# Kernel tuning notes

Hardware: AMD Instinct MI355X
Metric: run time of the kernel (lower is better)

Reference implementation:

```python
import jax, jax.numpy as jnp
import numpy as np

N = 12  # mmse_block_size
REAL_SIZE = N * (N + 1) // 2  # 78: diag + strict lower
IMAG_SIZE = N * (N - 1) // 2  # 66: strict lower only
ROWS, COLS = jnp.tril_indices(N)        # row-major (i, j<=i) matches torch loop order
ROWS_S, COLS_S = jnp.tril_indices(N, -1)  # strict lower, row-major, matches imag loop
DIAG_MASK = jnp.eye(N, dtype=bool)


def _mlp(x, W1, b1, W2, b2, W3, b3):
    h = jax.nn.relu(x @ W1 + b1)
    h = jax.nn.relu(h @ W2 + b2)
    return h @ W3 + b3


def _cholesky_outer(flat):
    # flat: [B, REAL_SIZE + IMAG_SIZE] -> [B, N, N] complex, L @ L^H
    B = flat.shape[0]
    L_real = jnp.zeros((B, N, N), flat.dtype).at[:, ROWS, COLS].set(flat[:, :REAL_SIZE])
    L_real = jnp.where(DIAG_MASK, jax.nn.softplus(L_real), L_real)
    L_imag = jnp.zeros((B, N, N), flat.dtype).at[:, ROWS_S, COLS_S].set(
        flat[:, REAL_SIZE:REAL_SIZE + IMAG_SIZE])
    L = L_real + 1j * L_imag
    return jnp.einsum('bij,bkj->bik', L, jnp.conj(L))


def setup_inputs() -> dict:
    key = jax.random.key(0)
    ks = jax.random.split(key, 13)
    L, H, OUT = 4096, 64, REAL_SIZE + IMAG_SIZE
    sc = lambda k, shp, fan: (jax.random.normal(k, shp, jnp.float32) / np.sqrt(fan))
    return {
        'channel_stats': jax.random.normal(ks[0], (8192, L), jnp.float32),
        'WC1': sc(ks[1], (L, H), L), 'bC1': jnp.zeros((H,), jnp.float32),
        'WC2': sc(ks[2], (H, H), H), 'bC2': jnp.zeros((H,), jnp.float32),
        'WC3': sc(ks[3], (H, OUT), H), 'bC3': jnp.zeros((OUT,), jnp.float32),
        'WR1': sc(ks[4], (L, H), L), 'bR1': jnp.zeros((H,), jnp.float32),
        'WR2': sc(ks[5], (H, H), H), 'bR2': jnp.zeros((H,), jnp.float32),
        'WR3': sc(ks[6], (H, OUT), H), 'bR3': jnp.zeros((OUT,), jnp.float32),
    }


def reference(channel_stats, WC1, bC1, WC2, bC2, WC3, bC3,
              WR1, bR1, WR2, bR2, WR3, bR3):
    C_flat = _mlp(channel_stats, WC1, bC1, WC2, bC2, WC3, bC3)
    R_flat = _mlp(channel_stats, WR1, bR1, WR2, bR2, WR3, bR3)
    C = _cholesky_outer(C_flat)
    R = _cholesky_outer(R_flat)
    return C, R
```

## Files before the change

### kernel.cpp

```cpp
#include <hip/hip_runtime.h>
#include <stdint.h>

#define M_ROWS 8192
#define K_DIM  4096
#define OUTD   144
#define PLANE  1179648
#define KCH    8
#define NSTEP  8

typedef __attribute__((ext_vector_type(4))) float  float4v;
typedef __attribute__((ext_vector_type(8))) short  short8v;

static __device__ __forceinline__ unsigned short f2bf(float f) {
    unsigned int u = __builtin_bit_cast(unsigned int, f);
    u += 0x7FFFu + ((u >> 16) & 1u);
    return (unsigned short)(u >> 16);
}

__global__ __launch_bounds__(256) void wt_kernel(
    const float* __restrict__ WC1, const float* __restrict__ WR1,
    unsigned short* __restrict__ Wt) {
    __shared__ float tile[64][65];
    const float* src = (blockIdx.y == 0) ? WC1 : WR1;
    const int k0 = blockIdx.x * 64;
    const int t = threadIdx.x;
    const int j = t & 63, qq = t >> 6;
#pragma unroll
    for (int p = 0; p < 16; ++p) {
        int i = p * 4 + qq;
        tile[i][j] = src[(size_t)(k0 + i) * 64 + j];
    }
    __syncthreads();
    const int tt  = blockIdx.x >> 1;
    const int ksb = (blockIdx.x & 1) * 2;
#pragma unroll
    for (int p = 0; p < 16; ++p) {
        int c = p * 256 + t;
        int e = c & 7, m = (c >> 3) & 15, q = (c >> 7) & 3;
        int ks_l = (c >> 9) & 1, w_l = (c >> 10) & 3;
        int kp = ks_l * 32 + q * 8 + e;
        int np = w_l * 16 + m;
        int wg = blockIdx.y * 4 + w_l;
        size_t dst = ((size_t)(wg * 32 + tt) * 4 + (ksb + ks_l)) * 512
                   + q * 128 + m * 8 + e;
        Wt[dst] = f2bf(tile[kp][np]);
    }
}


#define ISSUE_AX(S_, X0_, X1_, X2_, X3_)                       \
    do { const float* ap_ = xpw + (S_) * 64;                   \
         X0_ = *(const float4*)(ap_);                          \
         X1_ = *(const float4*)(ap_ + 4);                      \
         X2_ = *(const float4*)(ap_ + 32);                     \
         X3_ = *(const float4*)(ap_ + 36); } while (0)

#define STORE_AX(BUF_, X0_, X1_, X2_, X3_)                             \
    do { short8v s1_, s2_;                                             \
         s1_[0] = (short)f2bf((X0_).x); s1_[1] = (short)f2bf((X0_).y); \
         s1_[2] = (short)f2bf((X0_).z); s1_[3] = (short)f2bf((X0_).w); \
         s1_[4] = (short)f2bf((X1_).x); s1_[5] = (short)f2bf((X1_).y); \
         s1_[6] = (short)f2bf((X1_).z); s1_[7] = (short)f2bf((X1_).w); \
         s2_[0] = (short)f2bf((X2_).x); s2_[1] = (short)f2bf((X2_).y); \
         s2_[2] = (short)f2bf((X2_).z); s2_[3] = (short)f2bf((X2_).w); \
         s2_[4] = (short)f2bf((X3_).x); s2_[5] = (short)f2bf((X3_).y); \
         s2_[6] = (short)f2bf((X3_).z); s2_[7] = (short)f2bf((X3_).w); \
         *(short8v*)(awp + (BUF_) * 8192) = s1_;                       \
         *(short8v*)(awp + (BUF_) * 8192 + 512) = s2_; } while (0)

#define ISSUE_B2(S_, B0_, B1_)                                   \
    do { const unsigned short* bp_ = bpw + (size_t)(2 * (S_)) * 512; \
         B0_ = *(const short8v*)(bp_);                           \
         B1_ = *(const short8v*)(bp_ + 512); } while (0)

#define MFR2(BUF_, B0_, B1_)                                                   \
    do { _Pragma("unroll")                                                     \
         for (int rb = 0; rb < 8; ++rb) {                                      \
             const unsigned short* ab_ = Asm_ + (BUF_) * 8192 + rb * 1024 + lane * 8; \
             short8v a0_ = *(const short8v*)(ab_);                             \
             short8v a1_ = *(const short8v*)(ab_ + 512);                       \
             acc[rb] = __builtin_amdgcn_mfma_f32_16x16x32_bf16(a0_, B0_, acc[rb], 0, 0, 0); \
             acc[rb] = __builtin_amdgcn_mfma_f32_16x16x32_bf16(a1_, B1_, acc[rb], 0, 0, 0); \
         } } while (0)

__global__ __launch_bounds__(512, 4) void gemm1_kernel(
    const float* __restrict__ X, const unsigned short* __restrict__ Wt,
    float* __restrict__ PART) {
    __shared__ __align__(16) unsigned short Asm_[2 * 8192];

    const int tid  = threadIdx.x;
    const int lane = tid & 63;
    const int w    = tid >> 6;
    const int m    = lane & 15, q = lane >> 4;
    const int mt   = blockIdx.x & 63;
    const int kc   = blockIdx.x >> 6;
    const int r0   = mt * 128;

    const int srow = tid & 127, sq8 = tid >> 7;
    const float* xpw = X + (size_t)(r0 + srow) * K_DIM + kc * 512 + sq8 * 8;
    unsigned short* awp = Asm_ + (srow >> 4) * 1024 + (16 * sq8 + (srow & 15)) * 8;

    const unsigned short* bpw = Wt + (size_t)(w * 128 + kc * 16) * 512 + lane * 8;

    float4v acc[8];
#pragma unroll
    for (int rb = 0; rb < 8; ++rb) acc[rb] = (float4v){0.f, 0.f, 0.f, 0.f};

    float4 xa0, xa1, xa2, xa3;
    short8v bA0, bA1, bB0, bB1;

    ISSUE_AX(0, xa0, xa1, xa2, xa3);
    ISSUE_B2(0, bA0, bA1);

#pragma unroll 1
    for (int sp = 0; sp < NSTEP / 2; ++sp) {
        const int s = sp * 2;
        STORE_AX(0, xa0, xa1, xa2, xa3);
        ISSUE_AX(s + 1, xa0, xa1, xa2, xa3);
        asm volatile("s_waitcnt lgkmcnt(0)" ::: "memory");
        __builtin_amdgcn_s_barrier();
        __builtin_amdgcn_sched_barrier(0);
        ISSUE_B2(s + 1, bB0, bB1);
        MFR2(0, bA0, bA1);
        STORE_AX(1, xa0, xa1, xa2, xa3);
        if (s + 2 < NSTEP) ISSUE_AX(s + 2, xa0, xa1, xa2, xa3);
        asm volatile("s_waitcnt lgkmcnt(0)" ::: "memory");
        __builtin_amdgcn_s_barrier();
        __builtin_amdgcn_sched_barrier(0);
        if (s + 2 < NSTEP) ISSUE_B2(s + 2, bA0, bA1);
        MFR2(1, bB0, bB1);
    }

    {
        float* Pf = PART + (size_t)kc * (M_ROWS * 128);
        const int col = w * 16 + m;
#pragma unroll
        for (int rb = 0; rb < 8; ++rb)
#pragma unroll
            for (int i = 0; i < 4; ++i) {
                int grow = r0 + rb * 16 + q * 4 + i;
                Pf[(size_t)grow * 128 + col] = acc[rb][i];
            }
    }
}

__global__ __launch_bounds__(512, 6) void tail_kernel(
    const float* __restrict__ PART,
    const float* __restrict__ bC1, const float* __restrict__ bR1,
    const float* __restrict__ WC2, const float* __restrict__ bC2,
    const float* __restrict__ WR2, const float* __restrict__ bR2,
    const float* __restrict__ WC3, const float* __restrict__ bC3,
    const float* __restrict__ WR3, const float* __restrict__ bR3,
    unsigned int* __restrict__ O32) {
    __shared__ __align__(16) char smem[41216];
    float* hs  = (float*)smem;
    float* W2s = hs + 16 * 132;
    float* fl  = W2s;

    const int tid = threadIdx.x;
    const int r0  = blockIdx.x * 16;

    {
        int r = tid >> 5, c4 = tid & 31;
        const float* p0 = PART + (size_t)(r0 + r) * 128 + c4 * 4;
        float4 s = *(const float4*)(p0);
#pragma unroll
        for (int kc = 1; kc < KCH; ++kc) {
            float4 v = *(const float4*)(p0 + (size_t)kc * (M_ROWS * 128));
            s.x += v.x; s.y += v.y; s.z += v.z; s.w += v.w;
        }
        int c = c4 * 4;
        const float* bsrc = (c < 64) ? (bC1 + c) : (bR1 + (c - 64));
        s.x += bsrc[0]; s.y += bsrc[1]; s.z += bsrc[2]; s.w += bsrc[3];
        s.x = s.x > 0.f ? s.x : 0.f;  s.y = s.y > 0.f ? s.y : 0.f;
        s.z = s.z > 0.f ? s.z : 0.f;  s.w = s.w > 0.f ? s.w : 0.f;
        *(float4*)&hs[r * 132 + c] = s;
    }
#pragma unroll
    for (int p = 0; p < 4; ++p) {
        int fi = p * 512 + tid;
        int k = fi >> 5, c4 = fi & 31;
        int c = c4 * 4;
        const float* wsrc = (c < 64) ? (WC2 + (size_t)k * 64 + c)
                                     : (WR2 + (size_t)k * 64 + (c - 64));
        *(float4*)&W2s[k * 128 + c] = *(const float4*)wsrc;
    }
    __syncthreads();

    const int rg = tid >> 5;
    const int cg = tid & 31;
    const int koff2 = (cg < 16) ? 0 : 64;
    float acc2[4];
    {
        int c = cg * 4;
        const float* bsrc = (c < 64) ? (bC2 + c) : (bR2 + (c - 64));
#pragma unroll
        for (int j = 0; j < 4; ++j) acc2[j] = bsrc[j];
    }
    for (int k = 0; k < 64; ++k) {
        float4 wv = *(const float4*)&W2s[k * 128 + cg * 4];
        float a = hs[rg * 132 + koff2 + k];
        acc2[0] += a * wv.x; acc2[1] += a * wv.y;
        acc2[2] += a * wv.z; acc2[3] += a * wv.w;
    }
    float4 h2v;
    h2v.x = acc2[0] > 0.f ? acc2[0] : 0.f;
    h2v.y = acc2[1] > 0.f ? acc2[1] : 0.f;
    h2v.z = acc2[2] > 0.f ? acc2[2] : 0.f;
    h2v.w = acc2[3] > 0.f ? acc2[3] : 0.f;
    __syncthreads();
    *(float4*)&hs[rg * 132 + cg * 4] = h2v;
    __syncthreads();

#pragma unroll 1
    for (int pass = 0; pass < 3; ++pass) {
        int c = pass * 128 + cg * 4;
        if (c < 288) {
            const int brn = (c >= 144);
            const int cl = c - (brn ? 144 : 0);
            const float* W3 = brn ? WR3 : WC3;
            const float* b3 = brn ? bR3 : bC3;
            const int ko = brn ? 64 : 0;
            float a3[4];
#pragma unroll
            for (int j = 0; j < 4; ++j) a3[j] = b3[cl + j];
            for (int k = 0; k < 64; ++k) {
                float4 wv = *(const float4*)(W3 + (size_t)k * OUTD + cl);
                float a = hs[rg * 132 + ko + k];
                a3[0] += a * wv.x; a3[1] += a * wv.y;
                a3[2] += a * wv.z; a3[3] += a * wv.w;
            }
            float4 v; v.x = a3[0]; v.y = a3[1]; v.z = a3[2]; v.w = a3[3];
            *(float4*)&fl[rg * 288 + c] = v;
        }
    }
    __syncthreads();

    if (tid < 384) {
        int r = tid / 24, rem = tid % 24;
        int brn = rem / 12, ii = rem % 12;
        float* f = &fl[r * 288 + brn * 144];
        int d = ii * (ii + 1) / 2 + ii;
        float xv = f[d];
        f[d] = (xv > 20.f) ? xv : log1pf(expf(xv));
    }
    __syncthreads();

    for (int task = tid; task < 16 * 2 * 78; task += 512) {
        int r = task / 156, rem = task % 156;
        int brn = rem / 78, p = rem % 78;
        int i = 0;
        while (p >= (i + 1) * (i + 2) / 2) ++i;
        int j = p - i * (i + 1) / 2;
        const float* f = &fl[r * 288 + brn * 144];
        const float* g = f + 78;
        const int ti = i * (i + 1) / 2, tj = j * (j + 1) / 2;
        const int si = i * (i - 1) / 2, sj = j * (j - 1) / 2;
        float re = 0.f, im = 0.f;
        for (int k = 0; k <= j; ++k) {
            float ar_ = f[ti + k];
            float ai  = (k == i) ? 0.f : g[si + k];
            float br_ = f[tj + k];
            float bi  = (k == j) ? 0.f : g[sj + k];
            re += ar_ * br_ + ai * bi;
            im += ai * br_ - ar_ * bi;
        }
        unsigned int reb = (unsigned int)f2bf(re);
        unsigned int imb = (unsigned int)f2bf(im);
        unsigned int imn = (unsigned int)f2bf(-im);
        size_t base = brn ? (size_t)PLANE : 0;
        size_t q1 = (size_t)(r0 + r) * 144 + (size_t)(i * 12 + j);
        O32[base + q1] = imb | (reb << 16);
        if (i != j) {
            size_t q2 = (size_t)(r0 + r) * 144 + (size_t)(j * 12 + i);
            O32[base + q2] = imn | (reb << 16);
        }
    }
}

extern "C" void kernel_launch(void* const* d_in, const int* in_sizes, int n_in,
                              void* d_out, int out_size, void* d_ws, size_t ws_size,
                              hipStream_t stream) {
    const float* X   = (const float*)d_in[0];
    const float* WC1 = (const float*)d_in[1];
    const float* bC1 = (const float*)d_in[2];
    const float* WC2 = (const float*)d_in[3];
    const float* bC2 = (const float*)d_in[4];
    const float* WC3 = (const float*)d_in[5];
    const float* bC3 = (const float*)d_in[6];
    const float* WR1 = (const float*)d_in[7];
    const float* bR1 = (const float*)d_in[8];
    const float* WR2 = (const float*)d_in[9];
    const float* bR2 = (const float*)d_in[10];
    const float* WR3 = (const float*)d_in[11];
    const float* bR3 = (const float*)d_in[12];

    unsigned short* Wt  = (unsigned short*)d_ws;
    float* PART = (float*)((char*)d_ws + (2u << 20));
    unsigned int* O32 = (unsigned int*)d_out;

    wt_kernel<<<dim3(64, 2), 256, 0, stream>>>(WC1, WR1, Wt);
    gemm1_kernel<<<64 * KCH, 512, 0, stream>>>(X, Wt, PART);
    tail_kernel<<<M_ROWS / 16, 512, 0, stream>>>(
        PART, bC1, bR1, WC2, bC2, WR2, bR2, WC3, bC3, WR3, bR3, O32);
}
```

Measured before the change: 273.1 us.

## Move tail MLP layers 2 and 3 onto bf16 MFMA with split hi/lo precision

Layers 2 and 3 of the tail kernel now run on MFMA 16x16x32 bf16 instructions instead of scalar FMA loops. To keep accuracy close to fp32, activations and weights are each split into a bf16 high part and a bf16 low-part residual, and three MFMAs are issued per k-step. A new small kernel pre-packs W2/W3 into that split fragment layout in workspace, which removes the per-block W2 staging through LDS and the direct global W3 reads. The cost is an extra launch, changed LDS usage and occupancy (launch bounds go from 6 to 4), and slightly different numerics from dropping the lo*lo term.

Measured after the change: 258.8 us. -5.2%, faster.

```diff
diff --git a/kernel.cpp b/kernel.cpp
--- a/kernel.cpp
+++ b/kernel.cpp
@@ -10,11 +10,16 @@
 
 typedef __attribute__((ext_vector_type(4))) float  float4v;
 typedef __attribute__((ext_vector_type(8))) short  short8v;
+typedef __attribute__((ext_vector_type(4))) short  short4v;
 
 static __device__ __forceinline__ unsigned short f2bf(float f) {
     unsigned int u = __builtin_bit_cast(unsigned int, f);
     u += 0x7FFFu + ((u >> 16) & 1u);
     return (unsigned short)(u >> 16);
+}
+static __device__ __forceinline__ float bf2f(unsigned short h) {
+    unsigned int u = ((unsigned int)h) << 16;
+    return __builtin_bit_cast(float, u);
 }
 
 __global__ __launch_bounds__(256) void wt_kernel(
@@ -47,6 +52,31 @@
     }
 }
 
+__global__ __launch_bounds__(256) void w23_kernel(
+    const float* __restrict__ WC2, const float* __restrict__ WR2,
+    const float* __restrict__ WC3, const float* __restrict__ WR3,
+    unsigned short* __restrict__ W23f) {
+    for (int idx = blockIdx.x * 256 + threadIdx.x; idx < 52 * 512;
+         idx += 256 * 8) {
+        int slot = idx >> 9, r = idx & 511;
+        int qq = r >> 7, n = (r >> 3) & 15, e = r & 7;
+        float val;
+        if (slot < 16) {
+            int br = slot >> 3, nt = (slot >> 1) & 3, ks = slot & 1;
+            int k = ks * 32 + qq * 8 + e, col = nt * 16 + n;
+            val = (br ? WR2 : WC2)[k * 64 + col];
+        } else {
+            int g = slot - 16;
+            int br = g / 18, t2 = g % 18, nt = t2 >> 1, ks = t2 & 1;
+            int k = ks * 32 + qq * 8 + e, col = nt * 16 + n;
+            val = (br ? WR3 : WC3)[k * OUTD + col];
+        }
+        unsigned short hi = f2bf(val);
+        unsigned short lo = f2bf(val - bf2f(hi));
+        W23f[(size_t)(slot * 2) * 512 + r]     = hi;
+        W23f[(size_t)(slot * 2 + 1) * 512 + r] = lo;
+    }
+}
 
 #define ISSUE_AX(S_, X0_, X1_, X2_, X3_)                       \
     do { const float* ap_ = xpw + (S_) * 64;                   \
@@ -99,7 +129,6 @@
     const int srow = tid & 127, sq8 = tid >> 7;
     const float* xpw = X + (size_t)(r0 + srow) * K_DIM + kc * 512 + sq8 * 8;
     unsigned short* awp = Asm_ + (srow >> 4) * 1024 + (16 * sq8 + (srow & 15)) * 8;
-
     const unsigned short* bpw = Wt + (size_t)(w * 128 + kc * 16) * 512 + lane * 8;
 
     float4v acc[8];
@@ -144,95 +173,109 @@
     }
 }
 
-__global__ __launch_bounds__(512, 6) void tail_kernel(
-    const float* __restrict__ PART,
+#define MFMA16(A_, B_, C_) __builtin_amdgcn_mfma_f32_16x16x32_bf16(A_, B_, C_, 0, 0, 0)
+
+__global__ __launch_bounds__(512, 4) void tail_kernel(
+    const float* __restrict__ PART, const unsigned short* __restrict__ W23f,
     const float* __restrict__ bC1, const float* __restrict__ bR1,
-    const float* __restrict__ WC2, const float* __restrict__ bC2,
-    const float* __restrict__ WR2, const float* __restrict__ bR2,
-    const float* __restrict__ WC3, const float* __restrict__ bC3,
-    const float* __restrict__ WR3, const float* __restrict__ bR3,
+    const float* __restrict__ bC2, const float* __restrict__ bR2,
+    const float* __restrict__ bC3, const float* __restrict__ bR3,
     unsigned int* __restrict__ O32) {
-    __shared__ __align__(16) char smem[41216];
-    float* hs  = (float*)smem;
-    float* W2s = hs + 16 * 132;
-    float* fl  = W2s;
-
-    const int tid = threadIdx.x;
-    const int r0  = blockIdx.x * 16;
+    __shared__ __align__(16) unsigned short h1h[16 * 136];
+    __shared__ __align__(16) unsigned short h1l[16 * 136];
+    __shared__ __align__(16) unsigned short h2h[16 * 136];
+    __shared__ __align__(16) unsigned short h2l[16 * 136];
+    __shared__ __align__(16) float fl[16 * 288];
+
+    const int tid = threadIdx.x, lane = tid & 63, w = tid >> 6;
+    const int m = lane & 15, q = lane >> 4;
+    const int r0 = blockIdx.x * 16;
+
+    const int br2 = w >> 2, nt2 = w & 3;
+    const int slot2 = (br2 * 4 + nt2) * 2;
+    const unsigned short* wf = W23f + lane * 8;
+    short8v w2h0 = *(const short8v*)(wf + (size_t)((slot2 + 0) * 2 + 0) * 512);
+    short8v w2l0 = *(const short8v*)(wf + (size_t)((slot2 + 0) * 2 + 1) * 512);
+    short8v w2h1 = *(const short8v*)(wf + (size_t)((slot2 + 1) * 2 + 0) * 512);
+    short8v w2l1 = *(const short8v*)(wf + (size_t)((slot2 + 1) * 2 + 1) * 512);
+    const float bv2 = (br2 ? bR2 : bC2)[nt2 * 16 + m];
 
     {
         int r = tid >> 5, c4 = tid & 31;
         const float* p0 = PART + (size_t)(r0 + r) * 128 + c4 * 4;
-        float4 s = *(const float4*)(p0);
+        float4 s = *(const float4*)p0;
 #pragma unroll
         for (int kc = 1; kc < KCH; ++kc) {
             float4 v = *(const float4*)(p0 + (size_t)kc * (M_ROWS * 128));
             s.x += v.x; s.y += v.y; s.z += v.z; s.w += v.w;
         }
         int c = c4 * 4;
-        const float* bsrc = (c < 64) ? (bC1 + c) : (bR1 + (c - 64));
-        s.x += bsrc[0]; s.y += bsrc[1]; s.z += bsrc[2]; s.w += bsrc[3];
-        s.x = s.x > 0.f ? s.x : 0.f;  s.y = s.y > 0.f ? s.y : 0.f;
-        s.z = s.z > 0.f ? s.z : 0.f;  s.w = s.w > 0.f ? s.w : 0.f;
-        *(float4*)&hs[r * 132 + c] = s;
-    }
-#pragma unroll
-    for (int p = 0; p < 4; ++p) {
-        int fi = p * 512 + tid;
-        int k = fi >> 5, c4 = fi & 31;
-        int c = c4 * 4;
-        const float* wsrc = (c < 64) ? (WC2 + (size_t)k * 64 + c)
-                                     : (WR2 + (size_t)k * 64 + (c - 64));
-        *(float4*)&W2s[k * 128 + c] = *(const float4*)wsrc;
-    }
-    __syncthreads();
-
-    const int rg = tid >> 5;
-    const int cg = tid & 31;
-    const int koff2 = (cg < 16) ? 0 : 64;
-    float acc2[4];
+        const float* b1 = (c < 64) ? (bC1 + c) : (bR1 + (c - 64));
+        float v0 = fmaxf(s.x + b1[0], 0.f);
+        float v1 = fmaxf(s.y + b1[1], 0.f);
+        float v2 = fmaxf(s.z + b1[2], 0.f);
+        float v3 = fmaxf(s.w + b1[3], 0.f);
+        short4v hh, hl;
+        hh.x = (short)f2bf(v0); hl.x = (short)f2bf(v0 - bf2f((unsigned short)hh.x));
+        hh.y = (short)f2bf(v1); hl.y = (short)f2bf(v1 - bf2f((unsigned short)hh.y));
+        hh.z = (short)f2bf(v2); hl.z = (short)f2bf(v2 - bf2f((unsigned short)hh.z));
+        hh.w = (short)f2bf(v3); hl.w = (short)f2bf(v3 - bf2f((unsigned short)hh.w));
+        *(short4v*)&h1h[r * 136 + c] = hh;
+        *(short4v*)&h1l[r * 136 + c] = hl;
+    }
+    __syncthreads();
+
     {
-        int c = cg * 4;
-        const float* bsrc = (c < 64) ? (bC2 + c) : (bR2 + (c - 64));
-#pragma unroll
-        for (int j = 0; j < 4; ++j) acc2[j] = bsrc[j];
-    }
-    for (int k = 0; k < 64; ++k) {
-        float4 wv = *(const float4*)&W2s[k * 128 + cg * 4];
-        float a = hs[rg * 132 + koff2 + k];
-        acc2[0] += a * wv.x; acc2[1] += a * wv.y;
-        acc2[2] += a * wv.z; acc2[3] += a * wv.w;
-    }
-    float4 h2v;
-    h2v.x = acc2[0] > 0.f ? acc2[0] : 0.f;
-    h2v.y = acc2[1] > 0.f ? acc2[1] : 0.f;
-    h2v.z = acc2[2] > 0.f ? acc2[2] : 0.f;
-    h2v.w = acc2[3] > 0.f ? acc2[3] : 0.f;
-    __syncthreads();
-    *(float4*)&hs[rg * 132 + cg * 4] = h2v;
+        const unsigned short* ah = h1h + m * 136 + br2 * 64 + q * 8;
+        const unsigned short* al = h1l + m * 136 + br2 * 64 + q * 8;
+        short8v a_h0 = *(const short8v*)(ah);
+        short8v a_l0 = *(const short8v*)(al);
+        short8v a_h1 = *(const short8v*)(ah + 32);
+        short8v a_l1 = *(const short8v*)(al + 32);
+        float4v acc = {0.f, 0.f, 0.f, 0.f};
+        acc = MFMA16(a_h0, w2h0, acc);
+        acc = MFMA16(a_l0, w2h0, acc);
+        acc = MFMA16(a_h0, w2l0, acc);
+        acc = MFMA16(a_h1, w2h1, acc);
+        acc = MFMA16(a_l1, w2h1, acc);
+        acc = MFMA16(a_h1, w2l1, acc);
+        const int col = br2 * 64 + nt2 * 16 + m;
+#pragma unroll
+        for (int i = 0; i < 4; ++i) {
+            float v = fmaxf(acc[i] + bv2, 0.f);
+            unsigned short hi = f2bf(v);
+            h2h[(q * 4 + i) * 136 + col] = hi;
+            h2l[(q * 4 + i) * 136 + col] = f2bf(v - bf2f(hi));
+        }
+    }
     __syncthreads();
 
 #pragma unroll 1
-    for (int pass = 0; pass < 3; ++pass) {
-        int c = pass * 128 + cg * 4;
-        if (c < 288) {
-            const int brn = (c >= 144);
-            const int cl = c - (brn ? 144 : 0);
-            const float* W3 = brn ? WR3 : WC3;
-            const float* b3 = brn ? bR3 : bC3;
-            const int ko = brn ? 64 : 0;
-            float a3[4];
-#pragma unroll
-            for (int j = 0; j < 4; ++j) a3[j] = b3[cl + j];
-            for (int k = 0; k < 64; ++k) {
-                float4 wv = *(const float4*)(W3 + (size_t)k * OUTD + cl);
-                float a = hs[rg * 132 + ko + k];
-                a3[0] += a * wv.x; a3[1] += a * wv.y;
-                a3[2] += a * wv.z; a3[3] += a * wv.w;
-            }
-            float4 v; v.x = a3[0]; v.y = a3[1]; v.z = a3[2]; v.w = a3[3];
-            *(float4*)&fl[rg * 288 + c] = v;
-        }
+    for (int pair = w; pair < 18; pair += 8) {
+        const int br = (pair >= 9) ? 1 : 0;
+        const int nt = pair - br * 9;
+        const int slot3 = 16 + (br * 9 + nt) * 2;
+        short8v b_h0 = *(const short8v*)(wf + (size_t)((slot3 + 0) * 2 + 0) * 512);
+        short8v b_l0 = *(const short8v*)(wf + (size_t)((slot3 + 0) * 2 + 1) * 512);
+        short8v b_h1 = *(const short8v*)(wf + (size_t)((slot3 + 1) * 2 + 0) * 512);
+        short8v b_l1 = *(const short8v*)(wf + (size_t)((slot3 + 1) * 2 + 1) * 512);
+        const unsigned short* ah = h2h + m * 136 + br * 64 + q * 8;
+        const unsigned short* al = h2l + m * 136 + br * 64 + q * 8;
+        short8v a_h0 = *(const short8v*)(ah);
+        short8v a_l0 = *(const short8v*)(al);
+        short8v a_h1 = *(const short8v*)(ah + 32);
+        short8v a_l1 = *(const short8v*)(al + 32);
+        float4v acc = {0.f, 0.f, 0.f, 0.f};
+        acc = MFMA16(a_h0, b_h0, acc);
+        acc = MFMA16(a_l0, b_h0, acc);
+        acc = MFMA16(a_h0, b_l0, acc);
+        acc = MFMA16(a_h1, b_h1, acc);
+        acc = MFMA16(a_l1, b_h1, acc);
+        acc = MFMA16(a_h1, b_l1, acc);
+        const float bv3 = (br ? bR3 : bC3)[nt * 16 + m];
+#pragma unroll
+        for (int i = 0; i < 4; ++i)
+            fl[(q * 4 + i) * 288 + br * 144 + nt * 16 + m] = acc[i] + bv3;
     }
     __syncthreads();
 
@@ -295,12 +338,14 @@
     const float* WR3 = (const float*)d_in[11];
     const float* bR3 = (const float*)d_in[12];
 
-    unsigned short* Wt  = (unsigned short*)d_ws;
+    unsigned short* Wt   = (unsigned short*)d_ws;
+    unsigned short* W23f = (unsigned short*)((char*)d_ws + (1u << 20));
     float* PART = (float*)((char*)d_ws + (2u << 20));
     unsigned int* O32 = (unsigned int*)d_out;
 
     wt_kernel<<<dim3(64, 2), 256, 0, stream>>>(WC1, WR1, Wt);
+    w23_kernel<<<8, 256, 0, stream>>>(WC2, WR2, WC3, WR3, W23f);
     gemm1_kernel<<<64 * KCH, 512, 0, stream>>>(X, Wt, PART);
     tail_kernel<<<M_ROWS / 16, 512, 0, stream>>>(
-        PART, bC1, bR1, WC2, bC2, WR2, bR2, WC3, bC3, WR3, bR3, O32);
-}
+        PART, W23f, bC1, bR1, bC2, bR2, bC3, bR3, O32);
+}
```
